# Performance work log

Hardware: AMD Instinct MI355X
Metric: run time of the kernel (lower is better)

## Reference

```python
import jax, jax.numpy as jnp
import numpy as np

N = 100000
IN_PLANES = 64
OUT_PLANES = 64
SHARE = 8
NSAMPLE = 16


def setup_inputs() -> dict:
    key = jax.random.key(0)
    ks = jax.random.split(key, 20)
    f32 = jnp.float32
    s = lambda fan_in: 1.0 / np.sqrt(fan_in)
    inp = {}
    inp['p'] = jax.random.normal(ks[0], (N, 3), f32)
    inp['x'] = jax.random.normal(ks[1], (N, IN_PLANES), f32)
    inp['knn_idx'] = jax.random.randint(ks[2], (N, NSAMPLE), 0, N, jnp.int64)
    # channelMixMLPs01: Linear(3+in, nsample) -> ReLU -> Bilinear(ns, ns, ns)
    inp['W01'] = jax.random.uniform(ks[3], (3 + IN_PLANES, NSAMPLE), f32, -s(3 + IN_PLANES), s(3 + IN_PLANES))
    inp['b01'] = jnp.zeros((NSAMPLE,), f32)
    inp['Wbil'] = jax.random.uniform(ks[4], (NSAMPLE, NSAMPLE, NSAMPLE), f32, -s(NSAMPLE), s(NSAMPLE))
    inp['bbil'] = jnp.zeros((NSAMPLE,), f32)
    # linear_p: Linear(3,3) -> BN(3) -> ReLU -> Linear(3, out)
    inp['Wp1'] = jax.random.uniform(ks[5], (3, 3), f32, -s(3), s(3))
    inp['bp1'] = jnp.zeros((3,), f32)
    inp['bnp_s'] = jnp.ones((3,), f32)   # BN folded (inference): scale = gamma/sqrt(var+eps)
    inp['bnp_b'] = jnp.zeros((3,), f32)  # shift = beta - mean*scale
    inp['Wp2'] = jax.random.uniform(ks[6], (3, OUT_PLANES), f32, -s(3), s(3))
    inp['bp2'] = jnp.zeros((OUT_PLANES,), f32)
    # channelMixMLPs02
    mid = OUT_PLANES
    inp['W2a'] = jax.random.uniform(ks[7], (2 * NSAMPLE, mid), f32, -s(2 * NSAMPLE), s(2 * NSAMPLE))
    inp['bn2a_s'] = jnp.ones((mid,), f32)
    inp['bn2a_b'] = jnp.zeros((mid,), f32)
    inp['W2b'] = jax.random.uniform(ks[8], (mid, mid // SHARE), f32, -s(mid), s(mid))
    inp['bn2b_s'] = jnp.ones((mid // SHARE,), f32)
    inp['bn2b_b'] = jnp.zeros((mid // SHARE,), f32)
    inp['W2c'] = jax.random.uniform(ks[9], (mid // SHARE, OUT_PLANES // SHARE), f32, -s(mid // SHARE), s(mid // SHARE))
    inp['b2c'] = jnp.zeros((OUT_PLANES // SHARE,), f32)
    # channelMixMLPs03: Linear(in, out)
    inp['W3'] = jax.random.uniform(ks[10], (IN_PLANES, OUT_PLANES), f32, -s(IN_PLANES), s(IN_PLANES))
    inp['b3'] = jnp.zeros((OUT_PLANES,), f32)
    return inp


def reference(p, x, knn_idx, W01, b01, Wbil, bbil, Wp1, bp1, bnp_s, bnp_b,
              Wp2, bp2, W2a, bn2a_s, bn2a_b, W2b, bn2b_s, bn2b_b, W2c, b2c,
              W3, b3):
    n, k = knn_idx.shape
    out_planes = W3.shape[1]
    share = SHARE
    # queryandgroup(use_xyz=True): gather neighbors, relative xyz concat features
    p_r = p[knn_idx] - p[:, None, :]                      # [n,k,3]
    x_knn_in = jnp.concatenate([p_r, x[knn_idx]], -1)     # [n,k,3+in]
    xf = x_knn_in.reshape(n * k, -1)
    # channelMixMLPs01: Linear -> ReLU -> Bilinear(e, e)
    e = jax.nn.relu(xf @ W01 + b01)                       # [nk, ns]
    e = jnp.einsum('ni,oij,nj->no', e, Wbil, e) + bbil    # [nk, ns]
    # linear_p on relative coords
    pe = p_r.reshape(-1, 3) @ Wp1 + bp1
    pe = jax.nn.relu(pe * bnp_s + bnp_b)
    pe = pe @ Wp2 + bp2                                   # [nk, out]
    p_embed = pe.reshape(n, k, out_planes)
    # shrink_p: (n k (a b)) -> sum over a -> (nk, b=nsample)
    a = out_planes // k
    shrink = pe.reshape(n * k, a, k).sum(1)               # [nk, ns]
    ef = jnp.concatenate([e, shrink], -1)                 # [nk, 2*ns]
    # channelMixMLPs02
    h = jax.nn.relu((ef @ W2a) * bn2a_s + bn2a_b)
    h = jax.nn.relu((h @ W2b) * bn2b_s + bn2b_b)
    h = h @ W2c + b2c                                     # [nk, out/share]
    w = jax.nn.softmax(h.reshape(n, k, -1), axis=1)       # softmax over neighbors
    # channelMixMLPs03 then gather
    x_v = (x @ W3 + b3)[knn_idx]                          # [n,k,out]
    x_knn = (x_v + p_embed).reshape(n, k, share, out_planes // share)
    x_knn = (x_knn * w[:, :, None, :]).reshape(n, k, out_planes)
    x_out = x_knn.sum(1)                                  # [n,out]
    return (x_out, x_knn, knn_idx, p_r)
```

## Files before the change

### kernel.cpp

```cpp
#include <hip/hip_runtime.h>

#define NPTS 100000
#define NK   1600000

typedef __attribute__((ext_vector_type(8))) short bf16x8;
typedef __attribute__((ext_vector_type(4))) float f32x4;
typedef union { bf16x8 v; unsigned u[4]; } fragu;

#define MFMA(a,b,c) __builtin_amdgcn_mfma_f32_16x16x32_bf16((a),(b),(c),0,0,0)

#define WS_W01  0
#define WS_WBIL 1536
#define WS_W2A  5632
#define WS_W2B  7680
#define WS_WPE  8704
#define WS_BYTES 21504
#define WS_XBF   WS_BYTES
#define WS_YBF   (WS_BYTES + 12800000)
#define WS_NEED  (WS_BYTES + 25600000)

__device__ inline unsigned cvtpk(float lo, float hi) {
  unsigned r;
  asm("v_cvt_pk_bf16_f32 %0, %1, %2" : "=v"(r) : "v"(lo), "v"(hi));
  return r;
}
__device__ inline short bfr(float f) {
  unsigned u = __float_as_uint(f);
  u += 0x7fff + ((u >> 16) & 1);
  return (short)(u >> 16);
}
__device__ inline float bflo(unsigned u) { return __uint_as_float(u << 16); }
__device__ inline float bfhi(unsigned u) { return __uint_as_float(u & 0xffff0000u); }

template<int CTRL>
__device__ inline float fdpp(float x) {
  return __int_as_float(__builtin_amdgcn_update_dpp(
      0, __float_as_int(x), CTRL, 0xF, 0xF, true));
}
template<int XM>
__device__ inline float fswz(float x) {
  return __int_as_float(__builtin_amdgcn_ds_swizzle(
      __float_as_int(x), 0x1F | (XM << 10)));
}
__device__ inline unsigned bpermu(int src, unsigned v) {
  return (unsigned)__builtin_amdgcn_ds_bpermute(src << 2, (int)v);
}
__device__ inline float bpermf(int src, float v) {
  return __int_as_float(__builtin_amdgcn_ds_bpermute(src << 2, __float_as_int(v)));
}
__device__ inline int bpermi(int src, int v) {
  return __builtin_amdgcn_ds_bpermute(src << 2, v);
}

__global__ __launch_bounds__(256) void k_prep(
    const float* __restrict__ W01, const float* __restrict__ b01,
    const float* __restrict__ Wbil,
    const float* __restrict__ W2a, const float* __restrict__ W2b,
    const float* __restrict__ Wp2, const float* __restrict__ bp2,
    short* __restrict__ ws)
{
  const int t = threadIdx.x;
  for (int i = t; i < 3 * 512; i += 256) {
    int tt = i & 7, l = (i >> 3) & 63, kc = i >> 9;
    int o = l & 15, k = kc * 32 + ((l >> 4) << 3) + tt;
    float v = 0.f;
    if (k < 64) v = W01[(3 + k) * 16 + o];
    else if (k < 67) v = W01[(k - 64) * 16 + o];
    else if (k == 67) v = b01[o];
    ws[WS_W01 + i] = bfr(v);
  }
  for (int i = t; i < 8 * 512; i += 256) {
    int tt = i & 7, l = (i >> 3) & 63, kc = i >> 9;
    int o = l & 15, k = kc * 32 + ((l >> 4) << 3) + tt;
    ws[WS_WBIL + i] = bfr(Wbil[o * 256 + k]);
  }
  for (int i = t; i < 4 * 512; i += 256) {
    int tt = i & 7, l = (i >> 3) & 63, nt = i >> 9;
    int c = nt * 16 + (l & 15), k = ((l >> 4) << 3) + tt;
    ws[WS_W2A + i] = bfr(W2a[k * 64 + c]);
  }
  for (int i = t; i < 2 * 512; i += 256) {
    int tt = i & 7, l = (i >> 3) & 63, kc = i >> 9;
    int m = l & 15, k = kc * 32 + ((l >> 4) << 3) + tt;
    ws[WS_W2B + i] = bfr(m < 8 ? W2b[k * 8 + m] : 0.f);
  }
  for (int i = t; i < 4 * 512; i += 256) {
    int tt = i & 7, l = (i >> 3) & 63, nt = i >> 9;
    int c = nt * 16 + (l & 15), k = ((l >> 4) << 3) + tt;
    float v = 0.f;
    if (k < 3) v = Wp2[k * 64 + c]; else if (k == 3) v = bp2[c];
    ws[WS_WPE + i] = bfr(v);
  }
}

__global__ __launch_bounds__(256) void k_cvt(
    const float* __restrict__ x, unsigned* __restrict__ xb2)
{
  int t = blockIdx.x * 256 + threadIdx.x;
  f32x4 v = *(const f32x4*)&x[t * 4];
  uint2 o; o.x = cvtpk(v[0], v[1]); o.y = cvtpk(v[2], v[3]);
  *(uint2*)&xb2[t * 2] = o;
}

template<bool BF>
__global__ __launch_bounds__(256) void k_xw3(
    const float* __restrict__ x, const float* __restrict__ W3,
    const float* __restrict__ b3, void* __restrict__ yout)
{
  int t = blockIdx.x * 256 + threadIdx.x;
  int i = __builtin_amdgcn_readfirstlane(t >> 6);
  int c = t & 63;
  if (i >= NPTS) return;
  const float* xr = x + i * 64;
  float acc = b3[c];
#pragma unroll
  for (int k = 0; k < 64; ++k)
    acc = fmaf(xr[k], W3[k * 64 + c], acc);
  if constexpr (BF) ((short*)yout)[i * 64 + c] = bfr(acc);
  else              ((float*)yout)[i * 64 + c] = acc;
}

template<bool BF>
__global__ __launch_bounds__(256, 5) void k_main(
    const float* __restrict__ p, const float* __restrict__ x,
    const int* __restrict__ knn, const short* __restrict__ wsf,
    const float* __restrict__ Wp1, const float* __restrict__ bp1,
    const float* __restrict__ bnp_s, const float* __restrict__ bnp_b,
    const float* __restrict__ bbil,
    const float* __restrict__ bn2a_s, const float* __restrict__ bn2a_b,
    const float* __restrict__ bn2b_s, const float* __restrict__ bn2b_b,
    const float* __restrict__ W2c, const float* __restrict__ b2c,
    const float* __restrict__ Wp2, const float* __restrict__ bp2,
    const void* __restrict__ yv_, const void* __restrict__ xbf_,
    float* __restrict__ x_out, float* __restrict__ x_knn,
    float* __restrict__ knn_f, float* __restrict__ p_r)
{
  const int tid  = threadIdx.x;
  const int lane = tid & 63;
  const int mloc = lane & 15;
  const int kblk = lane >> 4;
  const int row  = blockIdx.x * 256 + tid;
  const int n    = row >> 4;
  const int j    = row & 15;
  const int idx  = knn[row];

  const float pr0 = p[idx * 3 + 0] - p[n * 3 + 0];
  const float pr1 = p[idx * 3 + 1] - p[n * 3 + 1];
  const float pr2 = p[idx * 3 + 2] - p[n * 3 + 2];

  float q0, q1, q2;
  {
    float v0 = bp1[0] + pr0 * Wp1[0] + pr1 * Wp1[3] + pr2 * Wp1[6];
    float v1 = bp1[1] + pr0 * Wp1[1] + pr1 * Wp1[4] + pr2 * Wp1[7];
    float v2 = bp1[2] + pr0 * Wp1[2] + pr1 * Wp1[5] + pr2 * Wp1[8];
    q0 = fmaxf(fmaf(v0, bnp_s[0], bnp_b[0]), 0.f);
    q1 = fmaxf(fmaf(v1, bnp_s[1], bnp_b[1]), 0.f);
    q2 = fmaxf(fmaf(v2, bnp_s[2], bnp_b[2]), 0.f);
  }

#define FR(off, idx_) (((const bf16x8*)wsf)[(off) / 8 + (idx_)])

  unsigned epk[4][2];
  {
    bf16x8 bw0 = FR(WS_W01, 0 * 64 + lane);
    bf16x8 bw1 = FR(WS_W01, 1 * 64 + lane);
    bf16x8 bw2 = FR(WS_W01, 2 * 64 + lane);
    const float4* x4 = (const float4*)x;
    const bf16x8* xb8 = (const bf16x8*)xbf_;
#pragma unroll
    for (int g = 0; g < 4; ++g) {
      const int src = g * 16 + mloc;
      int   ridx = bpermi(src, idx);
      float p0s  = bpermf(src, pr0);
      float p1s  = bpermf(src, pr1);
      float p2s  = bpermf(src, pr2);
      f32x4 acc = {0.f, 0.f, 0.f, 0.f};
      if constexpr (BF) {
        bf16x8 B0 = xb8[ridx * 8 + kblk];
        bf16x8 B1 = xb8[ridx * 8 + 4 + kblk];
        acc = MFMA(bw0, B0, acc);
        acc = MFMA(bw1, B1, acc);
      } else {
        {
          float4 xa = x4[ridx * 16 + kblk * 2];
          float4 xb = x4[ridx * 16 + kblk * 2 + 1];
          fragu B;
          B.u[0] = cvtpk(xa.x, xa.y); B.u[1] = cvtpk(xa.z, xa.w);
          B.u[2] = cvtpk(xb.x, xb.y); B.u[3] = cvtpk(xb.z, xb.w);
          acc = MFMA(bw0, B.v, acc);
        }
        {
          float4 xa = x4[ridx * 16 + 8 + kblk * 2];
          float4 xb = x4[ridx * 16 + 9 + kblk * 2];
          fragu B;
          B.u[0] = cvtpk(xa.x, xa.y); B.u[1] = cvtpk(xa.z, xa.w);
          B.u[2] = cvtpk(xb.x, xb.y); B.u[3] = cvtpk(xb.z, xb.w);
          acc = MFMA(bw1, B.v, acc);
        }
      }
      {
        fragu B;
        B.u[0] = (kblk == 0) ? cvtpk(p0s, p1s) : 0u;
        B.u[1] = (kblk == 0) ? cvtpk(p2s, 1.f) : 0u;
        B.u[2] = 0u; B.u[3] = 0u;
        acc = MFMA(bw2, B.v, acc);
      }
      epk[g][0] = cvtpk(fmaxf(acc[0], 0.f), fmaxf(acc[1], 0.f));
      epk[g][1] = cvtpk(fmaxf(acc[2], 0.f), fmaxf(acc[3], 0.f));
    }
  }

  unsigned h2p[4][2];
#pragma unroll
  for (int g = 0; g < 4; ++g) {
    float er[16];
    {
      unsigned a0 = bpermu(mloc,      epk[g][0]);
      unsigned a1 = bpermu(mloc,      epk[g][1]);
      unsigned b0 = bpermu(mloc + 16, epk[g][0]);
      unsigned b1 = bpermu(mloc + 16, epk[g][1]);
      unsigned c0 = bpermu(mloc + 32, epk[g][0]);
      unsigned c1 = bpermu(mloc + 32, epk[g][1]);
      unsigned d0 = bpermu(mloc + 48, epk[g][0]);
      unsigned d1 = bpermu(mloc + 48, epk[g][1]);
      er[0] = bflo(a0);  er[1] = bfhi(a0);  er[2]  = bflo(a1); er[3]  = bfhi(a1);
      er[4] = bflo(b0);  er[5] = bfhi(b0);  er[6]  = bflo(b1); er[7]  = bfhi(b1);
      er[8] = bflo(c0);  er[9] = bfhi(c0);  er[10] = bflo(c1); er[11] = bfhi(c1);
      er[12] = bflo(d0); er[13] = bfhi(d0); er[14] = bflo(d1); er[15] = bfhi(d1);
    }
    const int jhsel = kblk & 1, ihsel = kblk >> 1;
    float ej[8];
#pragma unroll
    for (int t = 0; t < 8; ++t) ej[t] = jhsel ? er[8 + t] : er[t];
    f32x4 acc2;
    {
      f32x4 bb = *(const f32x4*)&bbil[kblk * 4];
      acc2 = bb;
#pragma unroll
      for (int kc = 0; kc < 8; ++kc) {
        bf16x8 wb = FR(WS_WBIL, kc * 64 + lane);
        float ei = ihsel ? er[2 * kc + 1] : er[2 * kc];
        fragu B;
        B.u[0] = cvtpk(ei * ej[0], ei * ej[1]);
        B.u[1] = cvtpk(ei * ej[2], ei * ej[3]);
        B.u[2] = cvtpk(ei * ej[4], ei * ej[5]);
        B.u[3] = cvtpk(ei * ej[6], ei * ej[7]);
        acc2 = MFMA(wb, B.v, acc2);
      }
    }
    f32x4 shq;
    {
      const int src = g * 16 + mloc;
      float q0s = bpermf(src, q0);
      float q1s = bpermf(src, q1);
      float q2s = bpermf(src, q2);
      fragu B;
      B.u[0] = (kblk == 0) ? cvtpk(q0s, q1s) : 0u;
      B.u[1] = (kblk == 0) ? cvtpk(q2s, 1.f) : 0u;
      B.u[2] = 0u; B.u[3] = 0u;
      f32x4 z = {0.f, 0.f, 0.f, 0.f};
      f32x4 s0 = MFMA(FR(WS_WPE, 0 * 64 + lane), B.v, z);
      f32x4 s1 = MFMA(FR(WS_WPE, 1 * 64 + lane), B.v, z);
      f32x4 s2 = MFMA(FR(WS_WPE, 2 * 64 + lane), B.v, z);
      f32x4 s3 = MFMA(FR(WS_WPE, 3 * 64 + lane), B.v, z);
#pragma unroll
      for (int r = 0; r < 4; ++r) shq[r] = s0[r] + s1[r] + s2[r] + s3[r];
    }
    unsigned pe2_0 = cvtpk(acc2[0], acc2[1]);
    unsigned pe2_1 = cvtpk(acc2[2], acc2[3]);
    unsigned psh_0 = cvtpk(shq[0], shq[1]);
    unsigned psh_1 = cvtpk(shq[2], shq[3]);
    fragu Bef;
    {
      const int s1l = mloc + 32 * (kblk & 1);
      const int s2l = s1l + 16;
      unsigned a0 = bpermu(s1l, pe2_0);
      unsigned a1 = bpermu(s1l, pe2_1);
      unsigned a2 = bpermu(s2l, pe2_0);
      unsigned a3 = bpermu(s2l, pe2_1);
      unsigned b0 = bpermu(s1l, psh_0);
      unsigned b1 = bpermu(s1l, psh_1);
      unsigned b2 = bpermu(s2l, psh_0);
      unsigned b3 = bpermu(s2l, psh_1);
      const bool lo2 = (kblk < 2);
      Bef.u[0] = lo2 ? a0 : b0; Bef.u[1] = lo2 ? a1 : b1;
      Bef.u[2] = lo2 ? a2 : b2; Bef.u[3] = lo2 ? a3 : b3;
    }
    unsigned pha[8];
#pragma unroll
    for (int nt = 0; nt < 4; ++nt) {
      bf16x8 wa = FR(WS_W2A, nt * 64 + lane);
      f32x4 z = {0.f, 0.f, 0.f, 0.f};
      f32x4 c = MFMA(wa, Bef.v, z);
      f32x4 sA = *(const f32x4*)&bn2a_s[nt * 16 + kblk * 4];
      f32x4 bA = *(const f32x4*)&bn2a_b[nt * 16 + kblk * 4];
      float h0 = fmaxf(fmaf(c[0], sA[0], bA[0]), 0.f);
      float h1 = fmaxf(fmaf(c[1], sA[1], bA[1]), 0.f);
      float h2 = fmaxf(fmaf(c[2], sA[2], bA[2]), 0.f);
      float h3 = fmaxf(fmaf(c[3], sA[3], bA[3]), 0.f);
      pha[nt * 2 + 0] = cvtpk(h0, h1);
      pha[nt * 2 + 1] = cvtpk(h2, h3);
    }
    {
      const int sAl = mloc + 32 * (kblk & 1);
      const int sBl = sAl + 16;
      const bool lo2 = (kblk < 2);
      fragu B0, B1;
      {
        unsigned a0 = bpermu(sAl, pha[0]), a1 = bpermu(sAl, pha[1]);
        unsigned a2 = bpermu(sBl, pha[0]), a3 = bpermu(sBl, pha[1]);
        unsigned b0 = bpermu(sAl, pha[2]), b1 = bpermu(sAl, pha[3]);
        unsigned b2 = bpermu(sBl, pha[2]), b3 = bpermu(sBl, pha[3]);
        B0.u[0] = lo2 ? a0 : b0; B0.u[1] = lo2 ? a1 : b1;
        B0.u[2] = lo2 ? a2 : b2; B0.u[3] = lo2 ? a3 : b3;
      }
      {
        unsigned a0 = bpermu(sAl, pha[4]), a1 = bpermu(sAl, pha[5]);
        unsigned a2 = bpermu(sBl, pha[4]), a3 = bpermu(sBl, pha[5]);
        unsigned b0 = bpermu(sAl, pha[6]), b1 = bpermu(sAl, pha[7]);
        unsigned b2 = bpermu(sBl, pha[6]), b3 = bpermu(sBl, pha[7]);
        B1.u[0] = lo2 ? a0 : b0; B1.u[1] = lo2 ? a1 : b1;
        B1.u[2] = lo2 ? a2 : b2; B1.u[3] = lo2 ? a3 : b3;
      }
      f32x4 acc3 = {0.f, 0.f, 0.f, 0.f};
      acc3 = MFMA(FR(WS_W2B, 0 * 64 + lane), B0.v, acc3);
      acc3 = MFMA(FR(WS_W2B, 1 * 64 + lane), B1.v, acc3);
      f32x4 s = *(const f32x4*)&bn2b_s[(kblk & 1) * 4];
      f32x4 b = *(const f32x4*)&bn2b_b[(kblk & 1) * 4];
      float v0 = fmaxf(fmaf(acc3[0], s[0], b[0]), 0.f);
      float v1 = fmaxf(fmaf(acc3[1], s[1], b[1]), 0.f);
      float v2 = fmaxf(fmaf(acc3[2], s[2], b[2]), 0.f);
      float v3 = fmaxf(fmaf(acc3[3], s[3], b[3]), 0.f);
      h2p[g][0] = cvtpk(v0, v1);
      h2p[g][1] = cvtpk(v2, v3);
    }
  }

  unsigned hp0 = 0, hp1 = 0, hp2 = 0, hp3 = 0;
#pragma unroll
  for (int g = 0; g < 4; ++g) {
    unsigned t0 = bpermu(mloc,      h2p[g][0]);
    unsigned t1 = bpermu(mloc,      h2p[g][1]);
    unsigned t2 = bpermu(mloc + 16, h2p[g][0]);
    unsigned t3 = bpermu(mloc + 16, h2p[g][1]);
    const bool mine = (kblk == g);
    hp0 = mine ? t0 : hp0; hp1 = mine ? t1 : hp1;
    hp2 = mine ? t2 : hp2; hp3 = mine ? t3 : hp3;
  }
  float h2r[8];
  h2r[0] = bflo(hp0); h2r[1] = bfhi(hp0); h2r[2] = bflo(hp1); h2r[3] = bfhi(hp1);
  h2r[4] = bflo(hp2); h2r[5] = bfhi(hp2); h2r[6] = bflo(hp3); h2r[7] = bfhi(hp3);

  float h3[8];
#pragma unroll
  for (int b = 0; b < 8; ++b) h3[b] = b2c[b];
#pragma unroll
  for (int m = 0; m < 8; ++m) {
    float r = h2r[m];
#pragma unroll
    for (int b = 0; b < 8; ++b) h3[b] = fmaf(r, W2c[m * 8 + b], h3[b]);
  }
  float wv[8];
#pragma unroll
  for (int b = 0; b < 8; ++b) {
    float mx = h3[b];
    mx = fmaxf(mx, fdpp<0x128>(mx));
    mx = fmaxf(mx, fdpp<0x124>(mx));
    mx = fmaxf(mx, fdpp<0x122>(mx));
    mx = fmaxf(mx, fdpp<0x121>(mx));
    float ex = __expf(h3[b] - mx);
    float s = ex;
    s = s + fdpp<0x128>(s);
    s = s + fdpp<0x124>(s);
    s = s + fdpp<0x122>(s);
    s = s + fdpp<0x121>(s);
    wv[b] = ex * __builtin_amdgcn_rcpf(s);
  }

  float* xkrow = x_knn + (long long)row * 64;
  float xo[4];
#pragma unroll
  for (int h = 0; h < 2; ++h) {
    float v[32];
    if constexpr (BF) {
      const uint4* y4b = (const uint4*)yv_;
#pragma unroll
      for (int u2 = 0; u2 < 4; ++u2) {
        uint4 yw = y4b[idx * 8 + h * 4 + u2];
        unsigned wd[4] = {yw.x, yw.y, yw.z, yw.w};
#pragma unroll
        for (int half = 0; half < 2; ++half) {
          const int u = u2 * 2 + half;
          float comp[4] = {bflo(wd[half * 2]), bfhi(wd[half * 2]),
                           bflo(wd[half * 2 + 1]), bfhi(wd[half * 2 + 1])};
          f32x4 st;
#pragma unroll
          for (int cc = 0; cc < 4; ++cc) {
            const int c = h * 32 + u * 4 + cc;
            float pe = bp2[c] + q0 * Wp2[c] + q1 * Wp2[64 + c] + q2 * Wp2[128 + c];
            float val = (comp[cc] + pe) * wv[c & 7];
            v[u * 4 + cc] = val;
            st[cc] = val;
          }
          *(f32x4*)(xkrow + h * 32 + u * 4) = st;
        }
      }
    } else {
      const float4* y4 = (const float4*)yv_;
#pragma unroll
      for (int u = 0; u < 8; ++u) {
        float4 yw = y4[idx * 16 + h * 8 + u];
        float comp[4] = {yw.x, yw.y, yw.z, yw.w};
        f32x4 st;
#pragma unroll
        for (int cc = 0; cc < 4; ++cc) {
          const int c = h * 32 + u * 4 + cc;
          float pe = bp2[c] + q0 * Wp2[c] + q1 * Wp2[64 + c] + q2 * Wp2[128 + c];
          float val = (comp[cc] + pe) * wv[c & 7];
          v[u * 4 + cc] = val;
          st[cc] = val;
        }
        *(f32x4*)(xkrow + h * 32 + u * 4) = st;
      }
    }
    const bool b0 = (j & 1), b1 = (j & 2), b2 = (j & 4), b3 = (j & 8);
    float v1[16];
#pragma unroll
    for (int q = 0; q < 16; ++q) {
      float snd = b0 ? v[2 * q] : v[2 * q + 1];
      float rcv = fdpp<0xB1>(snd);
      v1[q] = (b0 ? v[2 * q + 1] : v[2 * q]) + rcv;
    }
    float v2[8];
#pragma unroll
    for (int r = 0; r < 8; ++r) {
      float snd = b1 ? v1[2 * r] : v1[2 * r + 1];
      float rcv = fdpp<0x4E>(snd);
      v2[r] = (b1 ? v1[2 * r + 1] : v1[2 * r]) + rcv;
    }
    float v3[4];
#pragma unroll
    for (int s = 0; s < 4; ++s) {
      float snd = b2 ? v2[2 * s] : v2[2 * s + 1];
      float rcv = fswz<4>(snd);
      v3[s] = (b2 ? v2[2 * s + 1] : v2[2 * s]) + rcv;
    }
    {
      float s0 = b3 ? v3[0] : v3[1];
      float s1 = b3 ? v3[2] : v3[3];
      float r0 = fswz<8>(s0);
      float r1 = fswz<8>(s1);
      xo[2 * h]     = (b3 ? v3[1] : v3[0]) + r0;
      xo[2 * h + 1] = (b3 ? v3[3] : v3[2]) + r1;
    }
  }
#pragma unroll
  for (int g = 0; g < 4; ++g)
    x_out[n * 64 + g * 16 + j] = xo[g];

  if (knn_f) {
    knn_f[row] = (float)idx;
    p_r[row * 3 + 0] = pr0;
    p_r[row * 3 + 1] = pr1;
    p_r[row * 3 + 2] = pr2;
  }
}

__global__ __launch_bounds__(256) void k_tail(
    const float* __restrict__ p, const int* __restrict__ knn,
    float* __restrict__ knn_f, float* __restrict__ p_r)
{
  int row = blockIdx.x * 256 + threadIdx.x;
  if (row >= NK) return;
  int n = row >> 4;
  int idx = knn[row];
  knn_f[row] = (float)idx;
  p_r[row * 3 + 0] = p[idx * 3 + 0] - p[n * 3 + 0];
  p_r[row * 3 + 1] = p[idx * 3 + 1] - p[n * 3 + 1];
  p_r[row * 3 + 2] = p[idx * 3 + 2] - p[n * 3 + 2];
}

extern "C" void kernel_launch(void* const* d_in, const int* in_sizes, int n_in,
                              void* d_out, int out_size, void* d_ws, size_t ws_size,
                              hipStream_t stream)
{
  const float* p    = (const float*)d_in[0];
  const float* x    = (const float*)d_in[1];
  const int*   knn  = (const int*)d_in[2];
  const float* W01  = (const float*)d_in[3];
  const float* b01  = (const float*)d_in[4];
  const float* Wbil = (const float*)d_in[5];
  const float* bbil = (const float*)d_in[6];
  const float* Wp1  = (const float*)d_in[7];
  const float* bp1  = (const float*)d_in[8];
  const float* bnps = (const float*)d_in[9];
  const float* bnpb = (const float*)d_in[10];
  const float* Wp2  = (const float*)d_in[11];
  const float* bp2  = (const float*)d_in[12];
  const float* W2a  = (const float*)d_in[13];
  const float* s2a  = (const float*)d_in[14];
  const float* b2a  = (const float*)d_in[15];
  const float* W2b  = (const float*)d_in[16];
  const float* s2b  = (const float*)d_in[17];
  const float* b2b  = (const float*)d_in[18];
  const float* W2c  = (const float*)d_in[19];
  const float* b2c  = (const float*)d_in[20];
  const float* W3   = (const float*)d_in[21];
  const float* b3   = (const float*)d_in[22];

  float* outF  = (float*)d_out;
  float* x_out = outF;
  float* x_knn = outF + 6400000;
  float* knn_f = outF + 108800000;
  float* p_r   = outF + 110400000;
  short* wsf   = (short*)d_ws;

  k_prep<<<1, 256, 0, stream>>>(W01, b01, Wbil, W2a, W2b, Wp2, bp2, wsf);

  if (ws_size >= (size_t)WS_NEED) {
    unsigned* xbf = (unsigned*)((char*)d_ws + WS_XBF);
    short*    ybf = (short*)((char*)d_ws + WS_YBF);
    k_cvt<<<6250, 256, 0, stream>>>(x, xbf);
    k_xw3<true><<<25000, 256, 0, stream>>>(x, W3, b3, ybf);
    k_main<true><<<6250, 256, 0, stream>>>(p, x, knn, wsf, Wp1, bp1, bnps, bnpb,
                                           bbil, s2a, b2a, s2b, b2b, W2c, b2c,
                                           Wp2, bp2, ybf, xbf, x_out, x_knn,
                                           knn_f, p_r);
  } else {
    float* y = knn_f;
    k_xw3<false><<<25000, 256, 0, stream>>>(x, W3, b3, y);
    k_main<false><<<6250, 256, 0, stream>>>(p, x, knn, wsf, Wp1, bp1, bnps, bnpb,
                                            bbil, s2a, b2a, s2b, b2b, W2c, b2c,
                                            Wp2, bp2, y, nullptr, x_out, x_knn,
                                            (float*)nullptr, (float*)nullptr);
    k_tail<<<6250, 256, 0, stream>>>(p, knn, knn_f, p_r);
  }
}
```

Before: 369.7 us.

## Permute MFMA weight row layouts so chained fragments need fewer bpermutes

Reorders the output rows of the bilinear, position-embedding and W2a weight fragments at prep time, so each MFMA's accumulator layout already matches the next MFMA's B-operand layout. This replaces eight ds_bpermute shuffles with two lane^32 exchanges for the concatenated feature, and removes sixteen bpermutes before the W2b MFMA entirely. The bias and BN parameter indexing is adjusted to follow the permuted rows. Launch bounds also rise from 5 to 8 waves per SIMD, which caps register use and may cause spills.

```diff
diff --git a/kernel.cpp b/kernel.cpp
--- a/kernel.cpp
+++ b/kernel.cpp
@@ -50,6 +50,13 @@
 }
 __device__ inline int bpermi(int src, int v) {
   return __builtin_amdgcn_ds_bpermute(src << 2, v);
+}
+
+__device__ inline int pb_m(int m) {
+  return 8 * ((m >> 2) & 1) + 4 * (m >> 3) + (m & 3);
+}
+__device__ inline int f2a(int nt, int m) {
+  return 8 * (m >> 2) + 4 * (nt & 1) + (m & 3) + 32 * (nt >> 1);
 }
 
 __global__ __launch_bounds__(256) void k_prep(
@@ -71,12 +78,12 @@
   }
   for (int i = t; i < 8 * 512; i += 256) {
     int tt = i & 7, l = (i >> 3) & 63, kc = i >> 9;
-    int o = l & 15, k = kc * 32 + ((l >> 4) << 3) + tt;
+    int o = pb_m(l & 15), k = kc * 32 + ((l >> 4) << 3) + tt;
     ws[WS_WBIL + i] = bfr(Wbil[o * 256 + k]);
   }
   for (int i = t; i < 4 * 512; i += 256) {
     int tt = i & 7, l = (i >> 3) & 63, nt = i >> 9;
-    int c = nt * 16 + (l & 15), k = ((l >> 4) << 3) + tt;
+    int c = f2a(nt, l & 15), k = ((l >> 4) << 3) + tt;
     ws[WS_W2A + i] = bfr(W2a[k * 64 + c]);
   }
   for (int i = t; i < 2 * 512; i += 256) {
@@ -86,7 +93,7 @@
   }
   for (int i = t; i < 4 * 512; i += 256) {
     int tt = i & 7, l = (i >> 3) & 63, nt = i >> 9;
-    int c = nt * 16 + (l & 15), k = ((l >> 4) << 3) + tt;
+    int c = nt * 16 + pb_m(l & 15), k = ((l >> 4) << 3) + tt;
     float v = 0.f;
     if (k < 3) v = Wp2[k * 64 + c]; else if (k == 3) v = bp2[c];
     ws[WS_WPE + i] = bfr(v);
@@ -121,7 +128,7 @@
 }
 
 template<bool BF>
-__global__ __launch_bounds__(256, 5) void k_main(
+__global__ __launch_bounds__(256, 8) void k_main(
     const float* __restrict__ p, const float* __restrict__ x,
     const int* __restrict__ knn, const short* __restrict__ wsf,
     const float* __restrict__ Wp1, const float* __restrict__ bp1,
@@ -210,6 +217,7 @@
     }
   }
 
+  const bool lo2 = (kblk < 2);
   unsigned h2p[4][2];
 #pragma unroll
   for (int g = 0; g < 4; ++g) {
@@ -234,8 +242,7 @@
     for (int t = 0; t < 8; ++t) ej[t] = jhsel ? er[8 + t] : er[t];
     f32x4 acc2;
     {
-      f32x4 bb = *(const f32x4*)&bbil[kblk * 4];
-      acc2 = bb;
+      acc2 = *(const f32x4*)&bbil[(kblk & 1) * 8 + (kblk >> 1) * 4];
 #pragma unroll
       for (int kc = 0; kc < 8; ++kc) {
         bf16x8 wb = FR(WS_WBIL, kc * 64 + lane);
@@ -272,19 +279,14 @@
     unsigned psh_1 = cvtpk(shq[2], shq[3]);
     fragu Bef;
     {
-      const int s1l = mloc + 32 * (kblk & 1);
-      const int s2l = s1l + 16;
-      unsigned a0 = bpermu(s1l, pe2_0);
-      unsigned a1 = bpermu(s1l, pe2_1);
-      unsigned a2 = bpermu(s2l, pe2_0);
-      unsigned a3 = bpermu(s2l, pe2_1);
-      unsigned b0 = bpermu(s1l, psh_0);
-      unsigned b1 = bpermu(s1l, psh_1);
-      unsigned b2 = bpermu(s2l, psh_0);
-      unsigned b3 = bpermu(s2l, psh_1);
-      const bool lo2 = (kblk < 2);
-      Bef.u[0] = lo2 ? a0 : b0; Bef.u[1] = lo2 ? a1 : b1;
-      Bef.u[2] = lo2 ? a2 : b2; Bef.u[3] = lo2 ? a3 : b3;
+      unsigned snd0 = lo2 ? psh_0 : pe2_0;
+      unsigned snd1 = lo2 ? psh_1 : pe2_1;
+      unsigned rcv0 = bpermu(lane ^ 32, snd0);
+      unsigned rcv1 = bpermu(lane ^ 32, snd1);
+      Bef.u[0] = lo2 ? pe2_0 : rcv0;
+      Bef.u[1] = lo2 ? pe2_1 : rcv1;
+      Bef.u[2] = lo2 ? rcv0 : psh_0;
+      Bef.u[3] = lo2 ? rcv1 : psh_1;
     }
     unsigned pha[8];
 #pragma unroll
@@ -292,8 +294,9 @@
       bf16x8 wa = FR(WS_W2A, nt * 64 + lane);
       f32x4 z = {0.f, 0.f, 0.f, 0.f};
       f32x4 c = MFMA(wa, Bef.v, z);
-      f32x4 sA = *(const f32x4*)&bn2a_s[nt * 16 + kblk * 4];
-      f32x4 bA = *(const f32x4*)&bn2a_b[nt * 16 + kblk * 4];
+      const int ab = 8 * kblk + 4 * (nt & 1) + 32 * (nt >> 1);
+      f32x4 sA = *(const f32x4*)&bn2a_s[ab];
+      f32x4 bA = *(const f32x4*)&bn2a_b[ab];
       float h0 = fmaxf(fmaf(c[0], sA[0], bA[0]), 0.f);
       float h1 = fmaxf(fmaf(c[1], sA[1], bA[1]), 0.f);
       float h2 = fmaxf(fmaf(c[2], sA[2], bA[2]), 0.f);
@@ -302,26 +305,9 @@
       pha[nt * 2 + 1] = cvtpk(h2, h3);
     }
     {
-      const int sAl = mloc + 32 * (kblk & 1);
-      const int sBl = sAl + 16;
-      const bool lo2 = (kblk < 2);
       fragu B0, B1;
-      {
-        unsigned a0 = bpermu(sAl, pha[0]), a1 = bpermu(sAl, pha[1]);
-        unsigned a2 = bpermu(sBl, pha[0]), a3 = bpermu(sBl, pha[1]);
-        unsigned b0 = bpermu(sAl, pha[2]), b1 = bpermu(sAl, pha[3]);
-        unsigned b2 = bpermu(sBl, pha[2]), b3 = bpermu(sBl, pha[3]);
-        B0.u[0] = lo2 ? a0 : b0; B0.u[1] = lo2 ? a1 : b1;
-        B0.u[2] = lo2 ? a2 : b2; B0.u[3] = lo2 ? a3 : b3;
-      }
-      {
-        unsigned a0 = bpermu(sAl, pha[4]), a1 = bpermu(sAl, pha[5]);
-        unsigned a2 = bpermu(sBl, pha[4]), a3 = bpermu(sBl, pha[5]);
-        unsigned b0 = bpermu(sAl, pha[6]), b1 = bpermu(sAl, pha[7]);
-        unsigned b2 = bpermu(sBl, pha[6]), b3 = bpermu(sBl, pha[7]);
-        B1.u[0] = lo2 ? a0 : b0; B1.u[1] = lo2 ? a1 : b1;
-        B1.u[2] = lo2 ? a2 : b2; B1.u[3] = lo2 ? a3 : b3;
-      }
+      B0.u[0] = pha[0]; B0.u[1] = pha[1]; B0.u[2] = pha[2]; B0.u[3] = pha[3];
+      B1.u[0] = pha[4]; B1.u[1] = pha[5]; B1.u[2] = pha[6]; B1.u[3] = pha[7];
       f32x4 acc3 = {0.f, 0.f, 0.f, 0.f};
       acc3 = MFMA(FR(WS_W2B, 0 * 64 + lane), B0.v, acc3);
       acc3 = MFMA(FR(WS_W2B, 1 * 64 + lane), B1.v, acc3);
```

Result: slower. 469.1 us (+26.9%).
